# Performance work log

Hardware: AMD Instinct MI355X
Metric: run time of the kernel (lower is better)

## Reference

```python
import jax, jax.numpy as jnp
import numpy as np

THETA = 10000.0
BATCH, SEQ_LEN, D_K = 32, 4096, 128


def setup_inputs() -> dict:
    key = jax.random.key(0)
    x = jax.random.normal(key, (BATCH, SEQ_LEN, D_K), dtype=jnp.float32)
    token_positions = jnp.arange(SEQ_LEN, dtype=jnp.int32)
    return {"x": x, "token_positions": token_positions}


def reference(x, token_positions):
    # Original builds a block-diagonal [seq, d_k, d_k] rotation matrix with
    # 2x2 blocks [[cos, sin], [-sin, cos]] and applies x @ R per position.
    # Equivalent pairwise form (same math, zero blocks dropped):
    #   out[2k]   = x[2k]*cos - x[2k+1]*sin
    #   out[2k+1] = x[2k]*sin + x[2k+1]*cos
    # with angle(i, k) = pos_i / theta ** (2k / d_k), k = 0..d_k/2-1.
    d = x.shape[-1]
    exponents = jnp.arange(0, d, 2, dtype=jnp.float32) / d            # [d/2]
    inv_freq = THETA ** (-exponents)                                   # [d/2]
    angles = token_positions.astype(jnp.float32)[:, None] * inv_freq  # [S, d/2]
    cos = jnp.cos(angles)
    sin = jnp.sin(angles)
    x_even = x[..., 0::2]  # [B, S, d/2]
    x_odd = x[..., 1::2]
    out_even = x_even * cos - x_odd * sin
    out_odd = x_even * sin + x_odd * cos
    # interleave back to [B, S, d]
    out = jnp.stack([out_even, out_odd], axis=-1).reshape(x.shape)
    return out
```

## Files before the change

kernel.cpp:

```cpp
#include <hip/hip_runtime.h>
#include <math.h>

#define BATCH   32
#define SEQLEN  4096
#define DK      128
#define NPAIR   (DK / 2)
#define NQUAD   (DK / 4)

#define LOG2_THETA 13.287712379549449f

__global__ void rope_build_table(const int* __restrict__ token_positions,
                                 float2* __restrict__ tab) {
    int t = blockIdx.x * blockDim.x + threadIdx.x;
    int i = t & (NPAIR - 1);
    int s = t >> 6;
    float p = (float)token_positions[s];
    float e = (float)(2 * i) * (1.0f / (float)DK);
    float inv_freq = exp2f(-e * LOG2_THETA);
    float ang = p * inv_freq;
    float sn, cs;
    sincosf(ang, &sn, &cs);
    tab[t] = make_float2(cs, sn);
}

__global__ void rope_apply(const float4* __restrict__ x,
                           const float4* __restrict__ tab,
                           float4* __restrict__ out,
                           int total_quads) {
    int t = blockIdx.x * blockDim.x + threadIdx.x;
    if (t >= total_quads) return;
    int j   = t & (NQUAD - 1);
    int row = t >> 5;
    int s   = row & (SEQLEN - 1);
    float4 v = x[t];
    float4 cz = tab[s * NQUAD + j];
    float4 o;
    o.x = v.x * cz.x - v.y * cz.y;
    o.y = v.x * cz.y + v.y * cz.x;
    o.z = v.z * cz.z - v.w * cz.w;
    o.w = v.z * cz.w + v.w * cz.z;
    out[t] = o;
}

__global__ void rope_fused(const float4* __restrict__ x,
                           const int* __restrict__ token_positions,
                           float4* __restrict__ out,
                           int total_quads) {
    int t = blockIdx.x * blockDim.x + threadIdx.x;
    if (t >= total_quads) return;
    int j   = t & (NQUAD - 1);
    int row = t >> 5;
    int s   = row & (SEQLEN - 1);
    float p = (float)token_positions[s];
    float4 v = x[t];
    float e0 = (float)(4 * j)     * (1.0f / (float)DK);
    float e1 = (float)(4 * j + 2) * (1.0f / (float)DK);
    float a0 = p * exp2f(-e0 * LOG2_THETA);
    float a1 = p * exp2f(-e1 * LOG2_THETA);
    float s0, c0, s1, c1;
    sincosf(a0, &s0, &c0);
    sincosf(a1, &s1, &c1);
    float4 o;
    o.x = v.x * c0 - v.y * s0;
    o.y = v.x * s0 + v.y * c0;
    o.z = v.z * c1 - v.w * s1;
    o.w = v.z * s1 + v.w * c1;
    out[t] = o;
}

extern "C" void kernel_launch(void* const* d_in, const int* in_sizes, int n_in,
                              void* d_out, int out_size, void* d_ws, size_t ws_size,
                              hipStream_t stream) {
    const float* x              = (const float*)d_in[0];
    const int*   token_positions = (const int*)d_in[1];
    float*       out            = (float*)d_out;

    const int total       = out_size;
    const int total_quads = total / 4;
    const size_t tab_bytes = (size_t)SEQLEN * NPAIR * sizeof(float2);

    if (ws_size >= tab_bytes) {
        float2* tab = (float2*)d_ws;
        {
            int n = SEQLEN * NPAIR;
            dim3 block(256), grid((n + 255) / 256);
            rope_build_table<<<grid, block, 0, stream>>>(token_positions, tab);
        }
        {
            dim3 block(256), grid((total_quads + 255) / 256);
            rope_apply<<<grid, block, 0, stream>>>((const float4*)x,
                                                   (const float4*)tab,
                                                   (float4*)out, total_quads);
        }
    } else {
        dim3 block(256), grid((total_quads + 255) / 256);
        rope_fused<<<grid, block, 0, stream>>>((const float4*)x, token_positions,
                                               (float4*)out, total_quads);
    }
}
```

Measured before the change: 114.6 us.

## Fuse RoPE into one kernel reusing sin/cos across batch with hardware trig

Replaces the table-build plus apply two-kernel path with a single kernel. Each thread computes the angle once for its (position, pair) slot and applies it to 8 batch rows, so the trig cost is spread over several rows. The kernel uses hardware exp2, sin and cos intrinsics with range reduction to [0,1) turns instead of the library sincosf. This removes the table write and read and one launch. The hardware trig may lose accuracy at large angles, and the fixed grid removes the size guard and the fallback path.

Result: faster. 112.2 us (-2.1%).

```diff
diff --git a/kernel.cpp b/kernel.cpp
--- a/kernel.cpp
+++ b/kernel.cpp
@@ -1,100 +1,65 @@
 #include <hip/hip_runtime.h>
 #include <math.h>
 
-#define BATCH   32
-#define SEQLEN  4096
-#define DK      128
-#define NPAIR   (DK / 2)
-#define NQUAD   (DK / 4)
+#define BATCH    32
+#define SEQLEN   4096
+#define DK       128
+#define NQUAD    (DK / 4)
+#define ROWQUADS (SEQLEN * NQUAD)
+#define BPT      8
 
 #define LOG2_THETA 13.287712379549449f
+#define INV_2PI    0.15915494309189535f
 
-__global__ void rope_build_table(const int* __restrict__ token_positions,
-                                 float2* __restrict__ tab) {
-    int t = blockIdx.x * blockDim.x + threadIdx.x;
-    int i = t & (NPAIR - 1);
-    int s = t >> 6;
-    float p = (float)token_positions[s];
-    float e = (float)(2 * i) * (1.0f / (float)DK);
-    float inv_freq = exp2f(-e * LOG2_THETA);
-    float ang = p * inv_freq;
-    float sn, cs;
-    sincosf(ang, &sn, &cs);
-    tab[t] = make_float2(cs, sn);
-}
+__global__ __launch_bounds__(256) void rope_fused_fast(
+    const float4* __restrict__ x,
+    const int*    __restrict__ pos,
+    float4*       __restrict__ out)
+{
+    int t     = blockIdx.x * blockDim.x + threadIdx.x;
+    int pid   = t & (ROWQUADS - 1);
+    int chunk = t >> 17;
+    int j     = pid & (NQUAD - 1);
+    int s     = pid >> 5;
 
-__global__ void rope_apply(const float4* __restrict__ x,
-                           const float4* __restrict__ tab,
-                           float4* __restrict__ out,
-                           int total_quads) {
-    int t = blockIdx.x * blockDim.x + threadIdx.x;
-    if (t >= total_quads) return;
-    int j   = t & (NQUAD - 1);
-    int row = t >> 5;
-    int s   = row & (SEQLEN - 1);
-    float4 v = x[t];
-    float4 cz = tab[s * NQUAD + j];
-    float4 o;
-    o.x = v.x * cz.x - v.y * cz.y;
-    o.y = v.x * cz.y + v.y * cz.x;
-    o.z = v.z * cz.z - v.w * cz.w;
-    o.w = v.z * cz.w + v.w * cz.z;
-    out[t] = o;
-}
+    float p = (float)pos[s];
 
-__global__ void rope_fused(const float4* __restrict__ x,
-                           const int* __restrict__ token_positions,
-                           float4* __restrict__ out,
-                           int total_quads) {
-    int t = blockIdx.x * blockDim.x + threadIdx.x;
-    if (t >= total_quads) return;
-    int j   = t & (NQUAD - 1);
-    int row = t >> 5;
-    int s   = row & (SEQLEN - 1);
-    float p = (float)token_positions[s];
-    float4 v = x[t];
-    float e0 = (float)(4 * j)     * (1.0f / (float)DK);
-    float e1 = (float)(4 * j + 2) * (1.0f / (float)DK);
-    float a0 = p * exp2f(-e0 * LOG2_THETA);
-    float a1 = p * exp2f(-e1 * LOG2_THETA);
-    float s0, c0, s1, c1;
-    sincosf(a0, &s0, &c0);
-    sincosf(a1, &s1, &c1);
-    float4 o;
-    o.x = v.x * c0 - v.y * s0;
-    o.y = v.x * s0 + v.y * c0;
-    o.z = v.z * c1 - v.w * s1;
-    o.w = v.z * s1 + v.w * c1;
-    out[t] = o;
+    float e0 = (float)j * (1.0f / 32.0f);
+    float e1 = e0 + (2.0f / 128.0f);
+    float f0 = __builtin_amdgcn_exp2f(-e0 * LOG2_THETA);
+    float f1 = __builtin_amdgcn_exp2f(-e1 * LOG2_THETA);
+
+    float r0 = p * f0 * INV_2PI;
+    float r1 = p * f1 * INV_2PI;
+    r0 = r0 - floorf(r0);
+    r1 = r1 - floorf(r1);
+    float s0 = __builtin_amdgcn_sinf(r0);
+    float c0 = __builtin_amdgcn_cosf(r0);
+    float s1 = __builtin_amdgcn_sinf(r1);
+    float c1 = __builtin_amdgcn_cosf(r1);
+
+    int base = pid + chunk * (BPT * ROWQUADS);
+    #pragma unroll
+    for (int i = 0; i < BPT; ++i) {
+        int idx = base + i * ROWQUADS;
+        float4 v = x[idx];
+        float4 o;
+        o.x = v.x * c0 - v.y * s0;
+        o.y = v.x * s0 + v.y * c0;
+        o.z = v.z * c1 - v.w * s1;
+        o.w = v.z * s1 + v.w * c1;
+        out[idx] = o;
+    }
 }
 
 extern "C" void kernel_launch(void* const* d_in, const int* in_sizes, int n_in,
                               void* d_out, int out_size, void* d_ws, size_t ws_size,
                               hipStream_t stream) {
-    const float* x              = (const float*)d_in[0];
-    const int*   token_positions = (const int*)d_in[1];
-    float*       out            = (float*)d_out;
+    const float* x   = (const float*)d_in[0];
+    const int*   pos = (const int*)d_in[1];
+    float*       out = (float*)d_out;
 
-    const int total       = out_size;
-    const int total_quads = total / 4;
-    const size_t tab_bytes = (size_t)SEQLEN * NPAIR * sizeof(float2);
-
-    if (ws_size >= tab_bytes) {
-        float2* tab = (float2*)d_ws;
-        {
-            int n = SEQLEN * NPAIR;
-            dim3 block(256), grid((n + 255) / 256);
-            rope_build_table<<<grid, block, 0, stream>>>(token_positions, tab);
-        }
-        {
-            dim3 block(256), grid((total_quads + 255) / 256);
-            rope_apply<<<grid, block, 0, stream>>>((const float4*)x,
-                                                   (const float4*)tab,
-                                                   (float4*)out, total_quads);
-        }
-    } else {
-        dim3 block(256), grid((total_quads + 255) / 256);
-        rope_fused<<<grid, block, 0, stream>>>((const float4*)x, token_positions,
-                                               (float4*)out, total_quads);
-    }
+    const int nthreads = (BATCH / BPT) * ROWQUADS;
+    dim3 block(256), grid(nthreads / 256);
+    rope_fused_fast<<<grid, block, 0, stream>>>((const float4*)x, pos, (float4*)out);
 }
```
